# Kernel tuning notes

Measured on AMD Instinct MI355X. Metric: run time of the kernel, lower is better.

The kernel has to match this reference:

```python
import math
import jax, jax.numpy as jnp
import numpy as np
from jax.scipy.linalg import cho_factor, cho_solve, block_diag

NUM_SENSORS = 64
T_STEPS = 2048
LOG2PI = float(np.log(2.0 * np.pi))

NCV_PROCESS_NOISE = np.array([[1.0/3.0, 0.0, 0.5, 0.0],
                              [0.0, 1.0/3.0, 0.0, 0.5],
                              [0.5, 0.0, 1.0, 0.0],
                              [0.0, 0.5, 0.0, 1.0]], dtype=np.float32)
NCV_TRANSITION_MATRIX = np.array([[1.0, 0.0, 1.0, 0.0],
                                  [0.0, 1.0, 0.0, 1.0],
                                  [0.0, 0.0, 1.0, 0.0],
                                  [0.0, 0.0, 0.0, 1.0]], dtype=np.float32)


def setup_inputs() -> dict:
    key = jax.random.key(0)
    k1, k2 = jax.random.split(key)
    track = jax.random.normal(k1, (T_STEPS, 2), dtype=jnp.float32)
    # positive covariance scales for the bias prior (torch param init ~ ones)
    bias_scales = jax.random.uniform(k2, (2,), jnp.float32, 0.5, 1.5)
    obs_noise = jnp.float32(0.7)
    trans_noise = jnp.float32(0.3)
    return {"track": track, "bias_scales": bias_scales,
            "obs_noise": obs_noise, "trans_noise": trans_noise}


def _hmm_forward(track, bias_scales, obs_noise, trans_noise, num_sensors):
    S = num_sensors
    OD = 2 * S           # obs_dim
    D = OD + 4           # augmented latent: [bias(OD); state(4)]
    T = track.shape[0]
    dt = track.dtype

    # observation matrix exactly as in torch source:
    # eye(4,2).expand(S,4,2).transpose(0,-1).reshape(4, OD)
    E = jnp.eye(4, 2, dtype=dt)
    Hobs = jnp.transpose(jnp.broadcast_to(E, (S, 4, 2)), (2, 1, 0)).reshape(4, OD)
    # augmented emission: y = bias + state @ Hobs  ->  H_aug z
    Haug = jnp.concatenate([jnp.eye(OD, dtype=dt), Hobs.T], axis=1)  # (OD, D)

    F = jnp.asarray(NCV_TRANSITION_MATRIX, dt)
    # trans scale_tril = trans_noise * chol(NCV_Q) -> cov = trans_noise^2 * NCV_Q
    Qs = (trans_noise ** 2) * jnp.asarray(NCV_PROCESS_NOISE, dt)
    A = block_diag(jnp.eye(OD, dtype=dt), F)                         # (D, D)
    Q = block_diag(jnp.zeros((OD, OD), dt), Qs)                      # (D, D)
    # obs scale_tril = obs_noise * I -> cov = obs_noise^2 * I
    R = (obs_noise ** 2) * jnp.eye(OD, dtype=dt)

    # bias prior covariance = diag(bias_scales interleaved per sensor)
    bias_var = jnp.broadcast_to(bias_scales, (S, 2)).reshape(-1)     # (OD,)
    m0 = jnp.zeros((D,), dt)
    P0 = jnp.diag(jnp.concatenate([bias_var, jnp.ones((4,), dt)]))

    # obs vector per step: x.expand(S,2).reshape(-1) (interleaved repeat)
    ys = jnp.broadcast_to(track[:, None, :], (T, S, 2)).reshape(T, OD)

    def step(carry, y):
        m, P, ll = carry
        # predict
        mp = A @ m
        Pp = A @ P @ A.T + Q
        # innovation
        HP = Haug @ Pp                      # (OD, D)
        Sm = HP @ Haug.T + R                # (OD, OD)
        cf = cho_factor(Sm, lower=True)
        v = y - Haug @ mp                   # (OD,)
        # update
        K = cho_solve(cf, HP)               # S^{-1} H Pp, (OD, D)
        m_new = mp + K.T @ v
        P_new = Pp - HP.T @ K
        P_new = 0.5 * (P_new + P_new.T)
        # log-likelihood of innovation
        logdet = 2.0 * jnp.sum(jnp.log(jnp.diag(cf[0])))
        quad = v @ cho_solve(cf, v)
        ll = ll - 0.5 * (OD * LOG2PI + logdet + quad)
        return (m_new, P_new, ll), None

    (mT, PT, ll), _ = jax.lax.scan(step, (m0, P0, jnp.zeros((), dt)), ys)
    # funsor's remaining Gaussian over (bias, state_T) has precision = inv(filtered cov)
    cfP = cho_factor(PT, lower=True)
    prec = cho_solve(cfP, jnp.eye(D, dtype=dt))
    return ll, prec


def reference(track, bias_scales, obs_noise, trans_noise):
    return _hmm_forward(track, bias_scales, obs_noise, trans_noise, NUM_SENSORS)
```

## Files before the change

kernel.cpp:

```cpp
#include <hip/hip_runtime.h>
#include <math.h>

#define L2PI 1.8378770664093454835606594728112
#define LN2  0.69314718055994530941723212145818
#define MAGIC 0x7E57C0DE

struct LP {
    float jFF, jFL, jFB, jLL, jLB, jBB;
    float hF, hL, hB, g, dm, de;
};

struct Cn { float qa, qb, qc, wa, wb, ri, Cstep; };

__device__ __forceinline__ float shf(float v, int s) { return __shfl(v, s, 64); }
__device__ __forceinline__ float sx (float v, int m) { return __shfl_xor(v, m, 64); }

__device__ __forceinline__ LP init_lane(float x0, float x1, const Cn& C, int i, int j) {
    LP P;
    float v = 0.0f;
    if (i == j) v = (i < 2) ? C.qa : C.qc;
    if ((i ^ j) == 2) v = C.wa;
    P.jFF = v;
    v = 0.0f;
    if (j == (i & 1))     v = (i < 2) ? -C.qa : -C.wa;
    if (j == (i & 1) + 2) v = (i < 2) ? -C.qb : -C.wb;
    P.jFL = v;
    P.jFB = 0.0f;
    v = 0.0f;
    if (i == j) v = ((i < 2) ? C.qa : C.qc) + (((i & 1) == 0) ? 2.0f*C.ri : 0.0f);
    if ((i ^ j) == 2) v = C.qb;
    P.jLL = v;
    P.jLB = (((i == 0) && (j < 2)) || ((i == 2) && (j >= 2))) ? C.ri : 0.0f;
    P.jBB = (i == j) ? C.ri : 0.0f;
    P.hF = 0.0f;
    P.hL = ((j & 1) == 0) ? C.ri * (x0 + x1) : 0.0f;
    P.hB = C.ri * ((j & 1) ? x1 : x0);
    P.g  = -C.ri * (x0*x0 + x1*x1) + C.Cstep;
    P.dm = 1.0f; P.de = 0.0f;
    return P;
}

__device__ __forceinline__ LP compose(const LP& P1, const LP& P2, int gb, int i, int j) {
    float hm = P1.hL + P2.hF;
    float Mb = P1.jLB + P2.jFB;
    float S  = P1.jLL + P2.jFF;
    float dm = P1.dm * P2.dm;
    float de = P1.de + P2.de;
    { int ex; dm = frexpf(dm, &ex); de += (float)ex; }
    const int r0 = (j == 0) ? 1 : 0;
    const int r1 = (j <= 1) ? 2 : 1;
    const int r2 = (j <= 2) ? 3 : 2;
    const int c0 = (i == 0) ? 1 : 0;
    const int c1 = (i <= 1) ? 2 : 1;
    const int c2 = (i <= 2) ? 3 : 2;
    float m00 = shf(S, gb + 4*r0 + c0), m01 = shf(S, gb + 4*r0 + c1), m02 = shf(S, gb + 4*r0 + c2);
    float m10 = shf(S, gb + 4*r1 + c0), m11 = shf(S, gb + 4*r1 + c1), m12 = shf(S, gb + 4*r1 + c2);
    float m20 = shf(S, gb + 4*r2 + c0), m21 = shf(S, gb + 4*r2 + c1), m22 = shf(S, gb + 4*r2 + c2);
    float d0 = fmaf(m11, m22, -m12*m21);
    float d1 = fmaf(m10, m22, -m12*m20);
    float d2 = fmaf(m10, m21, -m11*m20);
    float det3 = m00*d0 - m01*d1 + m02*d2;
    float adj = (((i + j) & 1) ? -det3 : det3);
    float sji = shf(S, gb + 4*j + i);
    float t = sji * adj;
    t += sx(t, 4); t += sx(t, 8);
    float det = t;
    dm *= det; { int ex; dm = frexpf(dm, &ex); de += (float)ex; }
    const float Si = adj * (1.0f / det);
    float sr[4], sc[4], f1r[4], f1T[4], f2c[4], f2T[4], mc[4], mT[4], hmc[4];
    #pragma unroll
    for (int r = 0; r < 4; ++r) {
        sr[r]  = shf(Si, gb + 4*i + r);
        sc[r]  = shf(Si, gb + 4*r + j);
        f1r[r] = shf(P1.jFL, gb + 4*i + r);
        f1T[r] = shf(P1.jFL, gb + 4*j + r);
        f2c[r] = shf(P2.jFL, gb + 4*r + j);
        f2T[r] = shf(P2.jFL, gb + 4*r + i);
        mc[r]  = shf(Mb, gb + 4*r + j);
        mT[r]  = shf(Mb, gb + 4*r + i);
        hmc[r] = shf(hm, gb + 5*r);
    }
    float A1 = 0.0f, C1 = 0.0f, B2 = 0.0f, v4i = 0.0f;
    #pragma unroll
    for (int r = 0; r < 4; ++r) {
        A1  = fmaf(f1r[r], sc[r], A1);
        C1  = fmaf(sr[r], mc[r], C1);
        B2  = fmaf(sr[r], f2c[r], B2);
        v4i = fmaf(sr[r], hmc[r], v4i);
    }
    float a1r[4], c1c[4], b2c[4], v4c[4];
    #pragma unroll
    for (int r = 0; r < 4; ++r) {
        a1r[r] = shf(A1, gb + 4*i + r);
        c1c[r] = shf(C1, gb + 4*r + j);
        b2c[r] = shf(B2, gb + 4*r + j);
        v4c[r] = shf(v4i, gb + 5*r);
    }
    float s_ff=0, s_fl=0, s_fb=0, s_ll=0, s_lb=0, s_bb=0, s_hf=0, s_hl=0, s_hb=0, s_g=0;
    #pragma unroll
    for (int r = 0; r < 4; ++r) {
        s_ff = fmaf(a1r[r], f1T[r], s_ff);
        s_fl = fmaf(a1r[r], f2c[r], s_fl);
        s_fb = fmaf(a1r[r], mc[r],  s_fb);
        s_ll = fmaf(f2T[r], b2c[r], s_ll);
        s_lb = fmaf(f2T[r], c1c[r], s_lb);
        s_bb = fmaf(mT[r],  c1c[r], s_bb);
        s_hf = fmaf(a1r[r], hmc[r], s_hf);
        s_hl = fmaf(f2c[r], v4c[r], s_hl);
        s_hb = fmaf(mc[r],  v4c[r], s_hb);
        s_g  = fmaf(hmc[r], v4c[r], s_g);
    }
    LP R;
    R.jFF = P1.jFF - s_ff;
    R.jFL = -s_fl;
    R.jFB = P1.jFB - s_fb;
    R.jLL = P2.jLL - s_ll;
    R.jLB = P2.jLB - s_lb;
    R.jBB = P1.jBB + P2.jBB - s_bb;
    R.hF  = P1.hF - shf(s_hf, gb + 5*j);
    R.hL  = P2.hL - s_hl;
    R.hB  = P1.hB + P2.hB - s_hb;
    R.g   = P1.g + P2.g + 2.0f*(float)L2PI + 0.5f*s_g;
    R.dm = dm; R.de = de;
    return R;
}

__device__ __forceinline__ LP fetchx(const LP& P, int m) {
    LP O;
    O.jFF = sx(P.jFF,m); O.jFL = sx(P.jFL,m); O.jFB = sx(P.jFB,m);
    O.jLL = sx(P.jLL,m); O.jLB = sx(P.jLB,m); O.jBB = sx(P.jBB,m);
    O.hF  = sx(P.hF,m);  O.hL  = sx(P.hL,m);  O.hB  = sx(P.hB,m);
    O.g   = sx(P.g,m);   O.dm  = sx(P.dm,m);  O.de  = sx(P.de,m);
    return O;
}
__device__ __forceinline__ LP csel(bool up, const LP& O, const LP& P) {
    LP A;
    A.jFF = up?O.jFF:P.jFF; A.jFL = up?O.jFL:P.jFL; A.jFB = up?O.jFB:P.jFB;
    A.jLL = up?O.jLL:P.jLL; A.jLB = up?O.jLB:P.jLB; A.jBB = up?O.jBB:P.jBB;
    A.hF  = up?O.hF :P.hF;  A.hL  = up?O.hL :P.hL;  A.hB  = up?O.hB :P.hB;
    A.g   = up?O.g  :P.g;   A.dm  = up?O.dm :P.dm;  A.de  = up?O.de :P.de;
    return A;
}
__device__ __forceinline__ void pot_store(float* p, const LP& P) {
    p[0]=P.jFF; p[1]=P.jFL; p[2]=P.jFB; p[3]=P.jLL; p[4]=P.jLB; p[5]=P.jBB;
    p[6]=P.hF;  p[7]=P.hL;  p[8]=P.hB;  p[9]=P.g;   p[10]=P.dm; p[11]=P.de;
}
__device__ __forceinline__ LP pot_load(const float* p) {
    LP P;
    P.jFF=p[0]; P.jFL=p[1]; P.jFB=p[2]; P.jLL=p[3]; P.jLB=p[4]; P.jBB=p[5];
    P.hF=p[6];  P.hL=p[7];  P.hB=p[8];  P.g=p[9];   P.dm=p[10]; P.de=p[11];
    return P;
}
__device__ __forceinline__ float cload(const float* p) {
    return __hip_atomic_load(p, __ATOMIC_RELAXED, __HIP_MEMORY_SCOPE_AGENT);
}
__device__ __forceinline__ LP pot_load_coh(const float* p) {
    LP P;
    P.jFF=cload(p+0); P.jFL=cload(p+1); P.jFB=cload(p+2);
    P.jLL=cload(p+3); P.jLB=cload(p+4); P.jBB=cload(p+5);
    P.hF=cload(p+6);  P.hL=cload(p+7);  P.hB=cload(p+8);
    P.g=cload(p+9);   P.dm=cload(p+10); P.de=cload(p+11);
    return P;
}

__global__ __launch_bounds__(512)
void hmm_fused(const float* __restrict__ track,
               const float* __restrict__ bias_scales,
               const float* __restrict__ obs_noise_p,
               const float* __restrict__ trans_noise_p,
               float* __restrict__ ws,
               float* __restrict__ out)
{
    __shared__ float pool[2][8][16][13];
    __shared__ float sTi[8][8];
    __shared__ float sA[4];
    __shared__ float sLL;
    const int tid = (int)threadIdx.x;
    const int l = tid & 63, w = tid >> 6;
    const int i = (l >> 2) & 3, j = l & 3, gb = l & 48, g = (l >> 4) & 3;
    const int gid = w * 4 + g;
    const int bid = (int)blockIdx.x;

    const double sg2d = (double)obs_noise_p[0] * (double)obs_noise_p[0];
    const double qn2d = (double)trans_noise_p[0] * (double)trans_noise_p[0];
    const double a00 = (double)bias_scales[0];
    const double a01 = (double)bias_scales[1];

    Cn C;
    C.qa = (float)(12.0/qn2d); C.qb = (float)(-6.0/qn2d); C.qc = (float)(4.0/qn2d);
    C.wa = (float)(6.0/qn2d);  C.wb = (float)(-2.0/qn2d);
    C.ri = (float)(32.0/sg2d);
    C.Cstep = (float)(-2.0*log(2.0*M_PI*sg2d/32.0) - 2.0*L2PI
                      - 0.5*(4.0*log(qn2d) - 2.0*log(12.0)));

    int* flags = (int*)(ws + 8192);

    {
        const int t0 = (bid * 32 + gid) * 2;
        LP P;
        #pragma unroll 1
        for (int op = 0; op < 6; ++op) {
            LP A, Bp;
            if (op == 0) {
                A  = init_lane(track[2*t0+0], track[2*t0+1], C, i, j);
                Bp = init_lane(track[2*t0+2], track[2*t0+3], C, i, j);
            } else if (op < 3) {
                const int m = 16 << (op - 1);
                LP O = fetchx(P, m);
                const bool up = (l & m) != 0;
                A  = csel(up, O, P);
                Bp = csel(up, P, O);
            } else {
                const int s = 1 << (op - 3);
                const int buf = (op - 3) & 1;
                if (l < 16) pot_store(&pool[buf][w][l][0], P);
                __syncthreads();
                LP O = pot_load(&pool[buf][w ^ s][l & 15][0]);
                const bool up = (w & s) != 0;
                A  = csel(up, O, P);
                Bp = csel(up, P, O);
            }
            P = compose(A, Bp, gb, i, j);
        }
        if (w == 0 && l < 16)
            pot_store(ws + ((size_t)bid * 16 + l) * 12, P);
        __threadfence();
        __syncthreads();
        if (tid == 0)
            __hip_atomic_store(&flags[bid * 32], MAGIC,
                               __ATOMIC_RELEASE, __HIP_MEMORY_SCOPE_AGENT);
    }
    if (bid != 0) return;

    if (tid < 32) {
        while (__hip_atomic_load(&flags[tid * 32],
                                 __ATOMIC_ACQUIRE, __HIP_MEMORY_SCOPE_AGENT) != MAGIC)
            __builtin_amdgcn_s_sleep(2);
    }
    __syncthreads();
    __threadfence();

    LP P = pot_load_coh(ws + ((size_t)gid * 16 + (l & 15)) * 12);
    #pragma unroll 1
    for (int op = 0; op < 5; ++op) {
        LP A, Bp;
        if (op < 2) {
            const int m = 16 << op;
            LP O = fetchx(P, m);
            const bool up = (l & m) != 0;
            A  = csel(up, O, P);
            Bp = csel(up, P, O);
        } else {
            const int s = 1 << (op - 2);
            const int buf = (op - 2) & 1;
            if (l < 16) pot_store(&pool[buf][w][l][0], P);
            __syncthreads();
            LP O = pot_load(&pool[buf][w ^ s][l & 15][0]);
            const bool up = (w & s) != 0;
            A  = csel(up, O, P);
            Bp = csel(up, P, O);
        }
        P = compose(A, Bp, gb, i, j);
    }

    if (w == 0) {
        const float a0i = (float)((i & 1) ? a01 : a00);
        P.jFF += (i == j) ? 1.0f : 0.0f;
        P.jBB += (i == j) ? 32.0f / a0i : 0.0f;
        P.g   += (float)(-4.0*L2PI + 2.0*log(32.0) - log(a00) - log(a01));
        float dm = P.dm, de = P.de;
        float S = P.jFF;
        const int r0 = (j == 0) ? 1 : 0;
        const int r1 = (j <= 1) ? 2 : 1;
        const int r2 = (j <= 2) ? 3 : 2;
        const int c0 = (i == 0) ? 1 : 0;
        const int c1 = (i <= 1) ? 2 : 1;
        const int c2 = (i <= 2) ? 3 : 2;
        float m00 = shf(S, gb + 4*r0 + c0), m01 = shf(S, gb + 4*r0 + c1), m02 = shf(S, gb + 4*r0 + c2);
        float m10 = shf(S, gb + 4*r1 + c0), m11 = shf(S, gb + 4*r1 + c1), m12 = shf(S, gb + 4*r1 + c2);
        float m20 = shf(S, gb + 4*r2 + c0), m21 = shf(S, gb + 4*r2 + c1), m22 = shf(S, gb + 4*r2 + c2);
        float d0 = fmaf(m11, m22, -m12*m21);
        float d1 = fmaf(m10, m22, -m12*m20);
        float d2 = fmaf(m10, m21, -m11*m20);
        float det3 = m00*d0 - m01*d1 + m02*d2;
        float adj = (((i + j) & 1) ? -det3 : det3);
        float sji = shf(S, gb + 4*j + i);
        float tdet = sji * adj;
        tdet += sx(tdet, 4); tdet += sx(tdet, 8);
        float det = tdet;
        dm *= det; { int ex; dm = frexpf(dm, &ex); de += (float)ex; }
        const float Si = adj * (1.0f / det);
        float sr[4], fr[4], fT[4], bc[4], bT[4], hfc[4];
        #pragma unroll
        for (int r = 0; r < 4; ++r) {
            sr[r]  = shf(Si, gb + 4*i + r);
            fr[r]  = shf(P.jFL, gb + 4*r + i);
            fT[r]  = shf(P.jFL, gb + 4*r + j);
            bc[r]  = shf(P.jFB, gb + 4*r + i);
            bT[r]  = shf(P.jFB, gb + 4*r + j);
            hfc[r] = shf(P.hF, gb + 5*r);
        }
        float YL = 0.0f, YB = 0.0f, yFi = 0.0f;
        #pragma unroll
        for (int r = 0; r < 4; ++r) {
            YL  = fmaf(sr[r], fT[r], YL);
            YB  = fmaf(sr[r], bT[r], YB);
            yFi = fmaf(sr[r], hfc[r], yFi);
        }
        float ylc[4], ybc[4], yfc[4];
        #pragma unroll
        for (int r = 0; r < 4; ++r) {
            ylc[r] = shf(YL, gb + 4*r + j);
            ybc[r] = shf(YB, gb + 4*r + j);
            yfc[r] = shf(yFi, gb + 5*r);
        }
        float s1 = 0.0f, s2 = 0.0f, s3 = 0.0f, sh1 = 0.0f, sh2 = 0.0f, qF = 0.0f;
        #pragma unroll
        for (int r = 0; r < 4; ++r) {
            s1  = fmaf(fr[r], ylc[r], s1);
            s2  = fmaf(fr[r], ybc[r], s2);
            s3  = fmaf(bc[r], ybc[r], s3);
            sh1 = fmaf(fT[r], yfc[r], sh1);
            sh2 = fmaf(bT[r], yfc[r], sh2);
            qF  = fmaf(hfc[r], yfc[r], qF);
        }
        float J8ss = P.jLL - s1;
        float J8sb = P.jLB - s2;
        float J8bb = P.jBB - s3;
        float h8s  = P.hL - sh1;
        float h8b  = P.hB - sh2;
        float g8   = P.g + 2.0f*(float)L2PI + 0.5f*qF;

        const int I = l >> 3, J = l & 7, i4 = I & 3, j4 = J & 3;
        float ss  = shf(J8ss, 4*i4 + j4);
        float sb  = shf(J8sb, 4*i4 + j4);
        float sbT = shf(J8sb, 4*j4 + i4);
        float bb  = shf(J8bb, 4*i4 + j4);
        float A8 = (I < 4) ? ((J < 4) ? ss : sb) : ((J < 4) ? sbT : bb);
        const float J8sav = A8;
        float h8v = (J < 4) ? shf(h8s, j4) : shf(h8b, j4);
        float h8r = (I < 4) ? shf(h8s, i4) : shf(h8b, i4);
        float K8 = (I == J) ? 1.0f : 0.0f;
        #pragma unroll 1
        for (int p = 0; p < 8; ++p) {
            float piv = shf(A8, 9*p);
            dm *= piv; { int ex; dm = frexpf(dm, &ex); de += (float)ex; }
            float ip = 1.0f / piv;
            float Ap = shf(A8, 8*p + J) * ip;
            float Kp = shf(K8, 8*p + J) * ip;
            float f  = shf(A8, 8*I + p);
            bool isp = (I == p);
            A8 = isp ? A8 * ip : fmaf(-f, Ap, A8);
            K8 = isp ? K8 * ip : fmaf(-f, Kp, K8);
        }
        float tq = h8r * K8 * h8v;
        tq += sx(tq,1); tq += sx(tq,2); tq += sx(tq,4);
        tq += sx(tq,8); tq += sx(tq,16); tq += sx(tq,32);

        double ll = (double)g8 + 4.0*L2PI
                    - 0.5*(log((double)dm) + (double)de*LN2) + 0.5*(double)tq;
        const double Td = 2048.0;
        const double c0d = sg2d/a00, c1d = sg2d/a01;
        ll += -31.0*(Td*(L2PI + log(sg2d)) + log((c0d+Td)/c0d))
              -31.0*(Td*(L2PI + log(sg2d)) + log((c1d+Td)/c1d))
              -2.0*Td*log(32.0);

        const float i32 = 1.0f/32.0f, irn = 0.176776695296637f;
        int a = (I >= 4) ? I - 4 : I + 4;
        int b = (J >= 4) ? J - 4 : J + 4;
        float scale = (I >= 4 && J >= 4) ? i32 : (((I >= 4) != (J >= 4)) ? irn : 1.0f);
        sTi[a][b] = J8sav * scale;
        if (l < 4) {
            double a0k = (l & 1) ? a01 : a00;
            sA[l] = (float)(a0k*sg2d/(sg2d + Td*a0k));
        }
        if (l == 0) sLL = (float)ll;
    }
    __syncthreads();

    const float inv32 = 1.0f/32.0f;
    const float invrn = 0.176776695296637f;
    const int total = 1 + 132*132;
    #pragma unroll 1
    for (int idx = tid; idx < total; idx += 512) {
        float v;
        if (idx == 0) {
            v = sLL;
        } else {
            int el = idx - 1;
            int r = el / 132;
            int cc = el - 132*r;
            if (r < 128) {
                int ki = ((r >> 6) << 1) | (r & 1);
                if (cc < 128) {
                    int kj = ((cc >> 6) << 1) | (cc & 1);
                    v = sTi[ki][kj] * inv32;
                    if (ki == kj) {
                        float ia = 1.0f / sA[ki];
                        v -= ia * inv32;
                        if (r == cc) v += ia;
                    }
                } else {
                    v = sTi[ki][cc - 124] * invrn;
                }
            } else {
                if (cc < 128) {
                    int kj = ((cc >> 6) << 1) | (cc & 1);
                    v = sTi[kj][r - 124] * invrn;
                } else {
                    v = sTi[r - 124][cc - 124];
                }
            }
        }
        out[idx] = v;
    }
}

extern "C" void kernel_launch(void* const* d_in, const int* in_sizes, int n_in,
                              void* d_out, int out_size, void* d_ws, size_t ws_size,
                              hipStream_t stream) {
    (void)in_sizes; (void)n_in; (void)out_size; (void)ws_size;
    const float* track       = (const float*)d_in[0];
    const float* bias_scales = (const float*)d_in[1];
    const float* obs_noise   = (const float*)d_in[2];
    const float* trans_noise = (const float*)d_in[3];
    float* out = (float*)d_out;
    float* ws  = (float*)d_ws;
    hipLaunchKernelGGL(hmm_fused, dim3(32), dim3(512), 0, stream,
                       track, bias_scales, obs_noise, trans_noise, ws, out);
}
```

Measured before the change: 97.28 us.

## Use last-block ticket reduction and halve block size with sequential leaf composes

```diff
diff --git a/kernel.cpp b/kernel.cpp
--- a/kernel.cpp
+++ b/kernel.cpp
@@ -3,7 +3,6 @@
 
 #define L2PI 1.8378770664093454835606594728112
 #define LN2  0.69314718055994530941723212145818
-#define MAGIC 0x7E57C0DE
 
 struct LP {
     float jFF, jFL, jFB, jLL, jLB, jBB;
@@ -163,7 +162,7 @@
     return P;
 }
 
-__global__ __launch_bounds__(512)
+__global__ __launch_bounds__(256)
 void hmm_fused(const float* __restrict__ track,
                const float* __restrict__ bias_scales,
                const float* __restrict__ obs_noise_p,
@@ -171,10 +170,11 @@
                float* __restrict__ ws,
                float* __restrict__ out)
 {
-    __shared__ float pool[2][8][16][13];
+    __shared__ float pool[2][4][16][13];
     __shared__ float sTi[8][8];
     __shared__ float sA[4];
     __shared__ float sLL;
+    __shared__ int sLast;
     const int tid = (int)threadIdx.x;
     const int l = tid & 63, w = tid >> 6;
     const int i = (l >> 2) & 3, j = l & 3, gb = l & 48, g = (l >> 4) & 3;
@@ -193,26 +193,28 @@
     C.Cstep = (float)(-2.0*log(2.0*M_PI*sg2d/32.0) - 2.0*L2PI
                       - 0.5*(4.0*log(qn2d) - 2.0*log(12.0)));
 
-    int* flags = (int*)(ws + 8192);
+    int* ticket = (int*)ws;
+    float* pots = ws + 64;
 
     {
-        const int t0 = (bid * 32 + gid) * 2;
-        LP P;
+        const int t0 = (bid * 16 + gid) * 4;
+        LP P = init_lane(track[2*t0+0], track[2*t0+1], C, i, j);
         #pragma unroll 1
-        for (int op = 0; op < 6; ++op) {
+        for (int op = 0; op < 7; ++op) {
             LP A, Bp;
-            if (op == 0) {
-                A  = init_lane(track[2*t0+0], track[2*t0+1], C, i, j);
-                Bp = init_lane(track[2*t0+2], track[2*t0+3], C, i, j);
-            } else if (op < 3) {
-                const int m = 16 << (op - 1);
+            if (op < 3) {
+                const int t = t0 + op + 1;
+                A  = P;
+                Bp = init_lane(track[2*t+0], track[2*t+1], C, i, j);
+            } else if (op < 5) {
+                const int m = 16 << (op - 3);
                 LP O = fetchx(P, m);
                 const bool up = (l & m) != 0;
                 A  = csel(up, O, P);
                 Bp = csel(up, P, O);
             } else {
-                const int s = 1 << (op - 3);
-                const int buf = (op - 3) & 1;
+                const int s = 1 << (op - 5);
+                const int buf = op - 5;
                 if (l < 16) pot_store(&pool[buf][w][l][0], P);
                 __syncthreads();
                 LP O = pot_load(&pool[buf][w ^ s][l & 15][0]);
@@ -223,26 +225,27 @@
             P = compose(A, Bp, gb, i, j);
         }
         if (w == 0 && l < 16)
-            pot_store(ws + ((size_t)bid * 16 + l) * 12, P);
+            pot_store(pots + ((size_t)bid * 16 + l) * 12, P);
         __threadfence();
         __syncthreads();
-        if (tid == 0)
-            __hip_atomic_store(&flags[bid * 32], MAGIC,
-                               __ATOMIC_RELEASE, __HIP_MEMORY_SCOPE_AGENT);
-    }
-    if (bid != 0) return;
-
-    if (tid < 32) {
-        while (__hip_atomic_load(&flags[tid * 32],
-                                 __ATOMIC_ACQUIRE, __HIP_MEMORY_SCOPE_AGENT) != MAGIC)
-            __builtin_amdgcn_s_sleep(2);
-    }
-    __syncthreads();
+        if (tid == 0) {
+            int old = __hip_atomic_fetch_add(ticket, 1, __ATOMIC_ACQ_REL,
+                                             __HIP_MEMORY_SCOPE_AGENT);
+            sLast = (old == 31) ? 1 : 0;
+        }
+        __syncthreads();
+        if (!sLast) return;
+    }
+
     __threadfence();
-
-    LP P = pot_load_coh(ws + ((size_t)gid * 16 + (l & 15)) * 12);
+    LP P;
+    {
+        LP Pa = pot_load_coh(pots + ((size_t)(2*gid    ) * 16 + (l & 15)) * 12);
+        LP Pb = pot_load_coh(pots + ((size_t)(2*gid + 1) * 16 + (l & 15)) * 12);
+        P = compose(Pa, Pb, gb, i, j);
+    }
     #pragma unroll 1
-    for (int op = 0; op < 5; ++op) {
+    for (int op = 0; op < 4; ++op) {
         LP A, Bp;
         if (op < 2) {
             const int m = 16 << op;
@@ -252,7 +255,7 @@
             Bp = csel(up, P, O);
         } else {
             const int s = 1 << (op - 2);
-            const int buf = (op - 2) & 1;
+            const int buf = op - 2;
             if (l < 16) pot_store(&pool[buf][w][l][0], P);
             __syncthreads();
             LP O = pot_load(&pool[buf][w ^ s][l & 15][0]);
@@ -382,7 +385,7 @@
     const float invrn = 0.176776695296637f;
     const int total = 1 + 132*132;
     #pragma unroll 1
-    for (int idx = tid; idx < total; idx += 512) {
+    for (int idx = tid; idx < total; idx += 256) {
         float v;
         if (idx == 0) {
             v = sLL;
@@ -426,6 +429,7 @@
     const float* trans_noise = (const float*)d_in[3];
     float* out = (float*)d_out;
     float* ws  = (float*)d_ws;
-    hipLaunchKernelGGL(hmm_fused, dim3(32), dim3(512), 0, stream,
+    hipMemsetAsync(d_ws, 0, 256, stream);
+    hipLaunchKernelGGL(hmm_fused, dim3(32), dim3(256), 0, stream,
                        track, bias_scales, obs_noise, trans_noise, ws, out);
 }
```

New measurement: 102.6 us. +5.5%, slower.
